# Performance work log

Measured on AMD Instinct MI355X. Metric: run time of the kernel, lower is better.

Reference implementation:

```python
import jax, jax.numpy as jnp
import numpy as np

NUM_HEADS = 6
NUM_TOKENS = 16
GROUP_SIZE = 32
PRO_COF = 0.4
CENTER_COF = 0.4


def _ln(x, g, b):
    m = jnp.mean(x, axis=-1, keepdims=True)
    v = jnp.var(x, axis=-1, keepdims=True)
    return (x - m) * jax.lax.rsqrt(v + 1e-5) * g + b


def _gelu(x):
    return jax.nn.gelu(x, approximate=False)


def _mhsa(x, qkv_w, proj_w, proj_b, mask=None):
    B, N, C = x.shape
    H = NUM_HEADS
    hd = C // H
    qkv = (x @ qkv_w.T).reshape(B, N, 3, H, hd).transpose(2, 0, 3, 1, 4)
    q, k, v = qkv[0], qkv[1], qkv[2]
    attn = jnp.einsum('bhnd,bhmd->bhnm', q, k) * (hd ** -0.5)
    if mask is not None:
        attn = attn + (mask * -100000.0)[:, None]  # additive mask, broadcast over heads
    attn = jax.nn.softmax(attn, axis=-1)
    out = jnp.einsum('bhnm,bhmd->bhnd', attn, v).transpose(0, 2, 1, 3).reshape(B, N, C)
    return out @ proj_w.T + proj_b


def _adapter(x, dw, db, uw, ub):
    # AdapterSuper: down-proj -> GELU -> up-proj + residual
    return _gelu(x @ dw.T + db) @ uw.T + ub + x


def _forward(x, mask, center1, center2, neighborhood, prompt_embeddings,
             n1_g, n1_b, qkv_w, proj_w, proj_b, n2_g, n2_b,
             fc1_w, fc1_b, fc2_w, fc2_b, ad_gate,
             ad_dw, ad_db, ad_uw, ad_ub, ad1_dw, ad1_db, ad1_uw, ad1_ub,
             bn_g, bn_b, a1_qkv_w, a1_proj_w, a1_proj_b, n3_g, n3_b,
             idx, center_idx):
    B, G1, C = x.shape
    T = NUM_TOKENS
    S = center2.shape[1]
    # mask_new: original mask in top-left, zeros for prompt slots
    mask = jnp.pad(mask, ((0, 0), (0, T), (0, T)))
    prompt = jnp.broadcast_to(prompt_embeddings[None], (B, T, C))
    x = jnp.concatenate([prompt, x], axis=1)                        # [B, T+G1, C]
    x = x + _mhsa(_ln(x, n1_g, n1_b), qkv_w, proj_w, proj_b, mask)
    h = _ln(x, n2_g, n2_b)
    x_fn = _gelu(h @ fc1_w.T + fc1_b) @ fc2_w.T + fc2_b             # MLP (drop_path=0 -> identity)
    x = ad_gate * _adapter(x_fn, ad_dw, ad_db, ad_uw, ad_ub) + x
    prompt = x[:, :T]
    xg = x[:, T:]
    prompt_x = jnp.concatenate([prompt, xg], axis=1)
    flat = prompt_x.reshape(B * (T + G1), C)
    x_neigh = flat[idx].reshape(B * S, GROUP_SIZE, C)               # irregular gather
    x_cent = flat[center_idx].reshape(B, S, C)
    # (neighborhood is normalized by its std in the original but never used afterwards)
    x_neigh = _mhsa(_ln(x_neigh, n3_g, n3_b), a1_qkv_w, a1_proj_w, a1_proj_b) + x_neigh
    knn = x_neigh.reshape(B, S, GROUP_SIZE, C)
    lc = jnp.max(knn, axis=2) + jnp.mean(knn, axis=2)               # if_maxmean=True pooling
    # eval-mode BatchNorm1d with running_mean=0, running_var=1, then GELU
    lc = _gelu(lc * bn_g * jax.lax.rsqrt(jnp.float32(1.0 + 1e-5)) + bn_b)
    vis_x = lc + CENTER_COF * x_cent                                # [B, S, C]
    # propagate: de_neighbors == S, so the sort is a no-op permutation and the
    # inverse-square-distance weighted sum runs over all centers.
    d = (jnp.sum(center1 ** 2, -1)[:, :, None] + jnp.sum(center2 ** 2, -1)[:, None, :]
         - 2.0 * jnp.einsum('bnc,bsc->bns', center1, center2))      # square_distance [B,G1,S]
    recip = 1.0 / (d + 1e-8)
    weight = recip / jnp.sum(recip, axis=-1, keepdims=True)
    interp = jnp.einsum('bns,bsc->bnc', weight, vis_x)
    new_x = xg + PRO_COF * interp
    x = jnp.concatenate([prompt, new_x], axis=1)
    x = _adapter(x, ad1_dw, ad1_db, ad1_uw, ad1_ub)
    return x[:, T:]


def setup_inputs() -> dict:
    key = jax.random.key(0)
    ks = iter(jax.random.split(key, 64))
    B, G, S, T, C, K = 32, 512, 128, NUM_TOKENS, 384, GROUP_SIZE
    H4, R = 4 * C, 16
    f32 = jnp.float32

    def rn(shape, s=0.02):
        return jax.random.normal(next(ks), shape, dtype=f32) * s

    return {
        'x': jax.random.normal(next(ks), (B, G, C), dtype=f32),
        'mask': (jax.random.uniform(next(ks), (B, G, G)) < 0.1).astype(f32),
        'center1': jax.random.normal(next(ks), (B, G, 3), dtype=f32),
        'center2': jax.random.normal(next(ks), (B, S, 3), dtype=f32),
        'neighborhood': jax.random.normal(next(ks), (B, S, K, 3), dtype=f32),
        'prompt_embeddings': rn((T, C)),
        'n1_g': jnp.ones((C,), f32), 'n1_b': jnp.zeros((C,), f32),
        'qkv_w': rn((3 * C, C)), 'proj_w': rn((C, C)), 'proj_b': jnp.zeros((C,), f32),
        'n2_g': jnp.ones((C,), f32), 'n2_b': jnp.zeros((C,), f32),
        'fc1_w': rn((H4, C)), 'fc1_b': jnp.zeros((H4,), f32),
        'fc2_w': rn((C, H4)), 'fc2_b': jnp.zeros((C,), f32),
        'ad_gate': jnp.full((1,), 0.5, f32),
        'ad_dw': rn((R, C)), 'ad_db': jnp.zeros((R,), f32),
        'ad_uw': rn((C, R)), 'ad_ub': jnp.zeros((C,), f32),
        'ad1_dw': rn((R, C)), 'ad1_db': jnp.zeros((R,), f32),
        'ad1_uw': rn((C, R)), 'ad1_ub': jnp.zeros((C,), f32),
        'bn_g': jnp.ones((C,), f32), 'bn_b': jnp.zeros((C,), f32),
        'a1_qkv_w': rn((3 * C, C)), 'a1_proj_w': rn((C, C)), 'a1_proj_b': jnp.zeros((C,), f32),
        'n3_g': jnp.ones((C,), f32), 'n3_b': jnp.zeros((C,), f32),
        'idx': jax.random.randint(next(ks), (B * S * K,), 0, B * (T + G)),
        'center_idx': jax.random.randint(next(ks), (B * S,), 0, B * (T + G)),
    }


def reference(x, mask, center1, center2, neighborhood, prompt_embeddings,
              n1_g, n1_b, qkv_w, proj_w, proj_b, n2_g, n2_b,
              fc1_w, fc1_b, fc2_w, fc2_b, ad_gate,
              ad_dw, ad_db, ad_uw, ad_ub, ad1_dw, ad1_db, ad1_uw, ad1_ub,
              bn_g, bn_b, a1_qkv_w, a1_proj_w, a1_proj_b, n3_g, n3_b,
              idx, center_idx):
    return _forward(x, mask, center1, center2, neighborhood, prompt_embeddings,
                    n1_g, n1_b, qkv_w, proj_w, proj_b, n2_g, n2_b,
                    fc1_w, fc1_b, fc2_w, fc2_b, ad_gate,
                    ad_dw, ad_db, ad_uw, ad_ub, ad1_dw, ad1_db, ad1_uw, ad1_ub,
                    bn_g, bn_b, a1_qkv_w, a1_proj_w, a1_proj_b, n3_g, n3_b,
                    idx, center_idx)
```

## Files before the change

kernel.cpp:

```cpp
#include <hip/hip_runtime.h>
#include <hip/hip_bf16.h>

#define Bq 32
#define Tq 16
#define Gq 512
#define NSEQ 528
#define Cq 384
#define Hq 6
#define Sq 128
#define Kg 32
#define ROWS (Bq*NSEQ)
#define LROWS (Bq*Sq*Kg)

typedef unsigned short u16;
typedef short bf16x8 __attribute__((ext_vector_type(8)));
typedef float f32x4  __attribute__((ext_vector_type(4)));

__device__ __forceinline__ float gelu_f(float x){
    return 0.5f * x * (1.0f + erff(x * 0.70710678118654752f));
}
__device__ __forceinline__ u16 f2b(float x){
    union { float f; unsigned u; } v; v.f = x;
    return (u16)((v.u + 0x7fffu + ((v.u >> 16) & 1u)) >> 16);
}
__device__ __forceinline__ float b2f(u16 h){
    union { float f; unsigned u; } v; v.u = ((unsigned)h) << 16; return v.f;
}

__device__ __forceinline__ void gload16(const u16* g, u16* l){
    __builtin_amdgcn_global_load_lds(
        (const __attribute__((address_space(1))) unsigned int*)(g),
        (__attribute__((address_space(3))) unsigned int*)(l), 16, 0, 0);
}

__global__ void __launch_bounds__(256) build_ln(const float* __restrict__ xin,
    const float* __restrict__ pe, const float* __restrict__ gw,
    const float* __restrict__ bw, float* __restrict__ X, u16* __restrict__ out)
{
    int w = threadIdx.x >> 6, lane = threadIdx.x & 63;
    int row = blockIdx.x*4 + w;
    if (row >= ROWS) return;
    int p = row % NSEQ; int b = row / NSEQ;
    const float* src = (p < Tq) ? (pe + (long)p*Cq)
                                : (xin + ((long)b*Gq + (p - Tq))*Cq);
    float v[6]; float s = 0.f, s2 = 0.f;
#pragma unroll
    for (int j = 0; j < 6; j++){ float x = src[lane + 64*j]; v[j] = x; s += x; s2 += x*x; }
#pragma unroll
    for (int m = 1; m < 64; m <<= 1){ s += __shfl_xor(s, m); s2 += __shfl_xor(s2, m); }
    float mean = s * (1.f/384.f);
    float var  = s2 * (1.f/384.f) - mean*mean;
    float rs   = rsqrtf(var + 1e-5f);
    float* xrow = X + (long)row*Cq;
    u16* orow = out + (long)row*Cq;
#pragma unroll
    for (int j = 0; j < 6; j++){
        int c = lane + 64*j;
        xrow[c] = v[j];
        orow[c] = f2b((v[j] - mean) * rs * gw[c] + bw[c]);
    }
}

__global__ void __launch_bounds__(256) conv6(const float* __restrict__ s0,
    const float* __restrict__ s1, const float* __restrict__ s2,
    const float* __restrict__ s3, const float* __restrict__ s4,
    const float* __restrict__ s5, u16* __restrict__ dst)
{
    long i = (long)blockIdx.x*256 + threadIdx.x;
    if (i >= 2359296) return;
    float v;
    if      (i <  442368) v = s0[i];
    else if (i <  589824) v = s1[i -  442368];
    else if (i < 1179648) v = s2[i -  589824];
    else if (i < 1769472) v = s3[i - 1179648];
    else if (i < 2211840) v = s4[i - 1769472];
    else                  v = s5[i - 2211840];
    dst[i] = f2b(v);
}

__global__ void __launch_bounds__(256) conv_mask(const float* __restrict__ m,
    u16* __restrict__ bias16)
{
    long i = (long)blockIdx.x*256 + threadIdx.x;
    if (i >= ((long)Bq*Gq*Gq >> 2)) return;
    float4 v = *(const float4*)(m + i*4);
    ushort4 r;
    r.x = f2b(-100000.0f * v.x);
    r.y = f2b(-100000.0f * v.y);
    r.z = f2b(-100000.0f * v.z);
    r.w = f2b(-100000.0f * v.w);
    *(ushort4*)(bias16 + i*4) = r;
}

__global__ void __launch_bounds__(256) ln_rows(const float* __restrict__ in,
    const float* __restrict__ gw, const float* __restrict__ bw,
    u16* __restrict__ out, int rows)
{
    int w = threadIdx.x >> 6, lane = threadIdx.x & 63;
    int row = blockIdx.x*4 + w;
    if (row >= rows) return;
    const float* xr = in + (long)row*Cq;
    float v[6]; float s = 0.f, s2 = 0.f;
#pragma unroll
    for (int j = 0; j < 6; j++){ float x = xr[lane + 64*j]; v[j] = x; s += x; s2 += x*x; }
#pragma unroll
    for (int m = 1; m < 64; m <<= 1){ s += __shfl_xor(s, m); s2 += __shfl_xor(s2, m); }
    float mean = s * (1.f/384.f);
    float var  = s2 * (1.f/384.f) - mean*mean;
    float rs   = rsqrtf(var + 1e-5f);
    u16* orow = out + (long)row*Cq;
#pragma unroll
    for (int j = 0; j < 6; j++){
        int c = lane + 64*j;
        orow[c] = f2b((v[j] - mean) * rs * gw[c] + bw[c]);
    }
}

__global__ void __launch_bounds__(512, 4) gemm_bf16(const u16* __restrict__ A,
    const u16* __restrict__ W, const float* __restrict__ bias,
    float* __restrict__ Cf, u16* __restrict__ Cb, int M, int N, int K, int epi)
{
    __shared__ u16 As0[128*32];
    __shared__ u16 As1[128*32];
    __shared__ u16 Ws0[128*32];
    __shared__ u16 Ws1[128*32];
    int t = threadIdx.x;
    int nx = gridDim.x;
    int nwg = nx * gridDim.y;
    int f = blockIdx.y*nx + blockIdx.x;
    int xcd = f & 7, i = f >> 3;
    int q = nwg >> 3, r = nwg & 7;
    int base = (xcd < r) ? xcd*(q+1) : r*(q+1) + (xcd - r)*q;
    int nf = base + i;
    int m0 = (nf / nx)*128, n0 = (nf % nx)*128;
    int wv = t >> 6, lane = t & 63;
    int wm = (wv >> 2)*64, wn = (wv & 3)*32;
    int fm = lane & 15;
    int fkp = (((lane >> 4) ^ ((fm >> 1) & 3)) & 3) * 8;
    int rs  = t >> 2;
    int kc8 = (((lane & 3) ^ ((lane >> 3) & 3))) * 8;
    f32x4 acc[4][2];
#pragma unroll
    for (int ii = 0; ii < 4; ii++)
#pragma unroll
        for (int j = 0; j < 2; j++) acc[ii][j] = (f32x4){0.f,0.f,0.f,0.f};

    auto STG = [&](u16* Ab, u16* Wb, int k0){
        gload16(A + (long)(m0 + rs)*K + k0 + kc8, Ab + wv*512);
        gload16(W + (long)(n0 + rs)*K + k0 + kc8, Wb + wv*512);
    };
    auto CMP = [&](const u16* Ab, const u16* Wb){
        bf16x8 af[4], bf[2];
#pragma unroll
        for (int im = 0; im < 4; im++) af[im] = *(const bf16x8*)&Ab[(wm + im*16 + fm)*32 + fkp];
#pragma unroll
        for (int in = 0; in < 2; in++) bf[in] = *(const bf16x8*)&Wb[(wn + in*16 + fm)*32 + fkp];
#pragma unroll
        for (int im = 0; im < 4; im++)
#pragma unroll
            for (int in = 0; in < 2; in++)
                acc[im][in] = __builtin_amdgcn_mfma_f32_16x16x32_bf16(af[im], bf[in], acc[im][in], 0, 0, 0);
    };

    int nt = K >> 5;
    STG(As0, Ws0, 0);
    __syncthreads();
    for (int kt = 0; kt < nt; kt += 2){
        STG(As1, Ws1, (kt+1)*32);
        CMP(As0, Ws0);
        __syncthreads();
        if (kt + 2 < nt) STG(As0, Ws0, (kt+2)*32);
        CMP(As1, Ws1);
        __syncthreads();
    }

    int lr = lane >> 4, lc = lane & 15;
#pragma unroll
    for (int im = 0; im < 4; im++){
#pragma unroll
        for (int in = 0; in < 2; in++){
#pragma unroll
            for (int r2 = 0; r2 < 4; r2++){
                int m = m0 + wm + im*16 + lr*4 + r2;
                int n = n0 + wn + in*16 + lc;
                float v = acc[im][in][r2];
                if (epi >= 1 && bias) v += bias[n];
                if (epi == 2) v = gelu_f(v);
                long off = (long)m*N + n;
                if (epi == 3) v += Cf[off];
                if (epi == 2 || epi == 4) Cb[off] = f2b(v);
                else                      Cf[off] = v;
            }
        }
    }
}

__global__ void __launch_bounds__(512, 4) gemm_pool(const u16* __restrict__ A,
    const u16* __restrict__ W, const float* __restrict__ bias,
    const int* __restrict__ idx, const int* __restrict__ cidx,
    const u16* __restrict__ X16, const float* __restrict__ bng,
    const float* __restrict__ bnb, float* __restrict__ vis, int K)
{
    __shared__ u16 As0[128*32];
    __shared__ u16 As1[128*32];
    __shared__ u16 Ws0[128*32];
    __shared__ u16 Ws1[128*32];
    __shared__ int idxl[128];
    __shared__ int cidxl[4];
    int t = threadIdx.x;
    int blkf = blockIdx.x;
    int xcd = blkf & 7, slot = blkf >> 3;
    int m0 = (xcd*128 + slot/3)*128;
    int n0 = (slot % 3)*128;
    if (t < 128) idxl[t] = idx[m0 + t];
    if (t < 4)   cidxl[t] = cidx[(m0 >> 5) + t];
    int wv = t >> 6, lane = t & 63;
    int wm = (wv >> 2)*64, wn = (wv & 3)*32;
    int fm = lane & 15;
    int fkp = (((lane >> 4) ^ ((fm >> 1) & 3)) & 3) * 8;
    int rs  = t >> 2;
    int kc8 = (((lane & 3) ^ ((lane >> 3) & 3))) * 8;
    f32x4 acc[4][2];
#pragma unroll
    for (int ii = 0; ii < 4; ii++)
#pragma unroll
        for (int j = 0; j < 2; j++) acc[ii][j] = (f32x4){0.f,0.f,0.f,0.f};

    auto STG = [&](u16* Ab, u16* Wb, int k0){
        gload16(A + (long)(m0 + rs)*K + k0 + kc8, Ab + wv*512);
        gload16(W + (long)(n0 + rs)*K + k0 + kc8, Wb + wv*512);
    };
    auto CMP = [&](const u16* Ab, const u16* Wb){
        bf16x8 af[4], bf[2];
#pragma unroll
        for (int im = 0; im < 4; im++) af[im] = *(const bf16x8*)&Ab[(wm + im*16 + fm)*32 + fkp];
#pragma unroll
        for (int in = 0; in < 2; in++) bf[in] = *(const bf16x8*)&Wb[(wn + in*16 + fm)*32 + fkp];
#pragma unroll
        for (int im = 0; im < 4; im++)
#pragma unroll
            for (int in = 0; in < 2; in++)
                acc[im][in] = __builtin_amdgcn_mfma_f32_16x16x32_bf16(af[im], bf[in], acc[im][in], 0, 0, 0);
    };

    int nt = K >> 5;
    STG(As0, Ws0, 0);
    __syncthreads();
    for (int kt = 0; kt < nt; kt += 2){
        STG(As1, Ws1, (kt+1)*32);
        CMP(As0, Ws0);
        __syncthreads();
        if (kt + 2 < nt) STG(As0, Ws0, (kt+2)*32);
        CMP(As1, Ws1);
        __syncthreads();
    }

    int lr = lane >> 4, lc = lane & 15;
#pragma unroll
    for (int in = 0; in < 2; in++){
        int c = n0 + wn + in*16 + lc;
        float pb = bias[c];
        float bg = bng[c], bb = bnb[c];
#pragma unroll
        for (int gl = 0; gl < 2; gl++){
            float vmax = -3e38f, vsum = 0.f;
#pragma unroll
            for (int i2 = 0; i2 < 2; i2++){
                int im = gl*2 + i2;
#pragma unroll
                for (int r = 0; r < 4; r++){
                    int rl = wm + im*16 + lr*4 + r;
                    float val = acc[im][in][r] + pb + b2f(X16[(long)idxl[rl]*Cq + c]);
                    vmax = fmaxf(vmax, val); vsum += val;
                }
            }
            vmax = fmaxf(vmax, __shfl_xor(vmax, 16)); vsum += __shfl_xor(vsum, 16);
            vmax = fmaxf(vmax, __shfl_xor(vmax, 32)); vsum += __shfl_xor(vsum, 32);
            if (lane < 16){
                int glb = (wm >> 5) + gl;
                float lcv = vmax + vsum*(1.f/32.f);
                float u = gelu_f(lcv*bg*0.9999950000374997f + bb);
                vis[((long)(m0 >> 5) + glb)*Cq + c] =
                    u + 0.4f*b2f(X16[(long)cidxl[glb]*Cq + c]);
            }
        }
    }
}

__global__ void __launch_bounds__(256) attn_mfma(const u16* __restrict__ QKVg,
    const u16* __restrict__ bias16, u16* __restrict__ out)
{
    __shared__ u16 Ks[32*72];
    __shared__ u16 Vt[64*40];
    __shared__ u16 Bs[64*36];
    __shared__ u16 Pb[4][16*40];
    int blk = blockIdx.x;
    int xcd = blk & 7; int r0 = blk >> 3;
    int bb = r0 & 3;  int rr = r0 >> 2;
    int h = rr % 6;   int qt = rr / 6;
    int b = xcd + 8*bb;
    int t = threadIdx.x; int w = t >> 6; int lane = t & 63;
    int fr  = lane & 15;
    int fko = (lane >> 4) * 8;
    int colj = lane & 15;
    int rgrp = (lane >> 4) * 4;
    int qb0 = qt*64;
    int q0 = qb0 + w*16;

    int qr = q0 + fr; int qrc = qr < NSEQ ? qr : NSEQ-1;
    const u16* qbase = QKVg + (long)(b*NSEQ + qrc)*1152 + h*64;
    bf16x8 aq0 = *(const bf16x8*)(qbase + fko);
    bf16x8 aq1 = *(const bf16x8*)(qbase + 32 + fko);

    f32x4 oacc[4];
#pragma unroll
    for (int d = 0; d < 4; d++) oacc[d] = (f32x4){0.f,0.f,0.f,0.f};
    float lsum[4] = {0.f, 0.f, 0.f, 0.f};

    int skey = t >> 3;
    int sd8  = (t & 7) * 8;
    int jswz = skey ^ ((t & 3) << 3);
    int brow = t >> 2;
    int bc8  = (t & 3) * 8;

    for (int kc = 0; kc < 17; kc++){
        __syncthreads();
        {
            int j = kc*32 + skey;
            bf16x8 kv = {0,0,0,0,0,0,0,0};
            bf16x8 vv = {0,0,0,0,0,0,0,0};
            if (j < NSEQ){
                const u16* kb = QKVg + (long)(b*NSEQ + j)*1152 + 384 + h*64 + sd8;
                kv = *(const bf16x8*)kb;
                vv = *(const bf16x8*)(kb + 384);
            }
            *(bf16x8*)&Ks[skey*72 + sd8] = kv;
#pragma unroll
            for (int e = 0; e < 8; e++) Vt[(sd8+e)*40 + jswz] = (u16)vv[e];
        }
        {
            int qi = qb0 + brow;
            int jj = kc*32 + bc8;
            uint4 bz = make_uint4(0u,0u,0u,0u);
            if (qi < Gq && jj < Gq)
                bz = *(const uint4*)(bias16 + ((long)b*Gq + qi)*Gq + jj);
            *(uint4*)&Bs[brow*36 + bc8] = bz;
        }
        __syncthreads();
        f32x4 s[2];
#pragma unroll
        for (int sub = 0; sub < 2; sub++){
            bf16x8 bk0 = *(const bf16x8*)&Ks[(sub*16 + fr)*72 + fko];
            bf16x8 bk1 = *(const bf16x8*)&Ks[(sub*16 + fr)*72 + 32 + fko];
            f32x4 z = (f32x4){0.f,0.f,0.f,0.f};
            z = __builtin_amdgcn_mfma_f32_16x16x32_bf16(aq0, bk0, z, 0, 0, 0);
            z = __builtin_amdgcn_mfma_f32_16x16x32_bf16(aq1, bk1, z, 0, 0, 0);
            s[sub] = z;
        }
#pragma unroll
        for (int sub = 0; sub < 2; sub++){
#pragma unroll
            for (int r = 0; r < 4; r++){
                int jj = kc*32 + sub*16 + colj;
                float sv = s[sub][r] * 0.125f
                         + b2f(Bs[(w*16 + rgrp + r)*36 + sub*16 + colj]);
                if (jj >= NSEQ) sv = -1e30f;
                float e = __expf(sv);
                lsum[r] += e;
                Pb[w][(rgrp + r)*40 + sub*16 + colj] = f2b(e);
            }
        }
        __syncthreads();
        bf16x8 ap = *(const bf16x8*)&Pb[w][fr*40 + fko];
#pragma unroll
        for (int d = 0; d < 4; d++){
            int D = d*16 + fr;
            int fkv = fko ^ (((D >> 3) & 3) << 3);
            bf16x8 bv = *(const bf16x8*)&Vt[D*40 + fkv];
            oacc[d] = __builtin_amdgcn_mfma_f32_16x16x32_bf16(ap, bv, oacc[d], 0, 0, 0);
        }
    }
#pragma unroll
    for (int r = 0; r < 4; r++){
#pragma unroll
        for (int mm = 1; mm < 16; mm <<= 1) lsum[r] += __shfl_xor(lsum[r], mm);
    }
#pragma unroll
    for (int r = 0; r < 4; r++){
        int qi = q0 + rgrp + r;
        if (qi < NSEQ){
            float inv = 1.0f / lsum[r];
#pragma unroll
            for (int d = 0; d < 4; d++)
                out[((long)(b*NSEQ + qi))*Cq + h*64 + d*16 + colj] = f2b(oacc[d][r]*inv);
        }
    }
}

__global__ void __launch_bounds__(256) adapter_fused(const float* __restrict__ xfn,
    const float* __restrict__ resid,
    const float* __restrict__ dw, const float* __restrict__ db,
    const float* __restrict__ uw, const float* __restrict__ ub,
    const float* __restrict__ gatep,
    const float* __restrict__ lng, const float* __restrict__ lnb,
    float* __restrict__ Xout, u16* __restrict__ x16out,
    u16* __restrict__ ln16, int rows)
{
    int w = threadIdx.x >> 6, lane = threadIdx.x & 63;
    int row = blockIdx.x*4 + w;
    if (row >= rows) return;
    const float* xr = xfn + (long)row*Cq;
    float xv[6];
#pragma unroll
    for (int j = 0; j < 6; j++) xv[j] = xr[lane + 64*j];
    float hid[16];
#pragma unroll
    for (int r = 0; r < 16; r++){
        const float* dr = dw + r*Cq;
        float p = 0.f;
#pragma unroll
        for (int j = 0; j < 6; j++) p += xv[j]*dr[lane + 64*j];
#pragma unroll
        for (int mm = 1; mm < 64; mm <<= 1) p += __shfl_xor(p, mm);
        hid[r] = gelu_f(p + db[r]);
    }
    float gate = gatep ? gatep[0] : 1.0f;
    float ov[6];
    float s = 0.f, s2 = 0.f;
#pragma unroll
    for (int j = 0; j < 6; j++){
        int c = lane + 64*j;
        const float* uc = uw + c*16;
        float a = 0.f;
#pragma unroll
        for (int r = 0; r < 16; r++) a += hid[r]*uc[r];
        float v = gate * (a + ub[c] + xv[j]);
        if (resid) v += resid[(long)row*Cq + c];
        ov[j] = v;
        Xout[(long)row*Cq + c] = v;
        if (x16out) x16out[(long)row*Cq + c] = f2b(v);
        s += v; s2 += v*v;
    }
    if (lng){
#pragma unroll
        for (int m = 1; m < 64; m <<= 1){ s += __shfl_xor(s, m); s2 += __shfl_xor(s2, m); }
        float mean = s * (1.f/384.f);
        float var  = s2 * (1.f/384.f) - mean*mean;
        float rs   = rsqrtf(var + 1e-5f);
        u16* orow = ln16 + (long)row*Cq;
#pragma unroll
        for (int j = 0; j < 6; j++){
            int c = lane + 64*j;
            orow[c] = f2b((ov[j] - mean)*rs*lng[c] + lnb[c]);
        }
    }
}

__global__ void __launch_bounds__(256) local_attn(const u16* __restrict__ QKVg,
    const int* __restrict__ idx, u16* __restrict__ aout16)
{
    __shared__ u16 Qs[32*72];
    __shared__ u16 Ksm[32*72];
    __shared__ u16 Vt[64*40];
    __shared__ float sc[32*36];
    __shared__ u16 Pa[32*40];
    __shared__ float linv[32];
    __shared__ int rows[32];
    int g = blockIdx.x;
    int t = threadIdx.x;
    int w = t >> 6, lane = t & 63;
    if (t < 32) rows[t] = idx[g*Kg + t];
    __syncthreads();
    int srow = t & 31;
    int d8   = (t >> 5) * 8;
    int jswz = srow ^ (((t >> 5) & 3) << 3);
    int fr = lane & 15, fko = (lane >> 4)*8;
    int colj = lane & 15, rgrp = (lane >> 4)*4;
    int it = w >> 1, jt = w & 1;
    int smrow = w*8 + (lane >> 3);
    int smc   = (lane & 7) * 4;

    for (int h = 0; h < Hq; h++){
        {
            const u16* base = QKVg + (long)rows[srow]*1152 + h*64 + d8;
            bf16x8 qv = *(const bf16x8*)(base);
            bf16x8 kv = *(const bf16x8*)(base + 384);
            bf16x8 vv = *(const bf16x8*)(base + 768);
            *(bf16x8*)&Qs[srow*72 + d8]  = qv;
            *(bf16x8*)&Ksm[srow*72 + d8] = kv;
#pragma unroll
            for (int e = 0; e < 8; e++) Vt[(d8+e)*40 + jswz] = (u16)vv[e];
        }
        __syncthreads();
        {
            bf16x8 a0 = *(const bf16x8*)&Qs[(it*16+fr)*72 + fko];
            bf16x8 a1 = *(const bf16x8*)&Qs[(it*16+fr)*72 + 32 + fko];
            bf16x8 b0 = *(const bf16x8*)&Ksm[(jt*16+fr)*72 + fko];
            bf16x8 b1 = *(const bf16x8*)&Ksm[(jt*16+fr)*72 + 32 + fko];
            f32x4 z = (f32x4){0.f,0.f,0.f,0.f};
            z = __builtin_amdgcn_mfma_f32_16x16x32_bf16(a0, b0, z, 0, 0, 0);
            z = __builtin_amdgcn_mfma_f32_16x16x32_bf16(a1, b1, z, 0, 0, 0);
#pragma unroll
            for (int r = 0; r < 4; r++)
                sc[(it*16 + rgrp + r)*36 + jt*16 + colj] = z[r]*0.125f;
        }
        __syncthreads();
        {
            float4 s4 = *(const float4*)&sc[smrow*36 + smc];
            float mx = fmaxf(fmaxf(s4.x, s4.y), fmaxf(s4.z, s4.w));
#pragma unroll
            for (int mm = 1; mm < 8; mm <<= 1) mx = fmaxf(mx, __shfl_xor(mx, mm));
            float p0 = __expf(s4.x - mx), p1 = __expf(s4.y - mx);
            float p2 = __expf(s4.z - mx), p3 = __expf(s4.w - mx);
            float sm = p0 + p1 + p2 + p3;
#pragma unroll
            for (int mm = 1; mm < 8; mm <<= 1) sm += __shfl_xor(sm, mm);
            if ((lane & 7) == 0) linv[smrow] = 1.0f / sm;
            Pa[smrow*40 + smc + 0] = f2b(p0);
            Pa[smrow*40 + smc + 1] = f2b(p1);
            Pa[smrow*40 + smc + 2] = f2b(p2);
            Pa[smrow*40 + smc + 3] = f2b(p3);
        }
        __syncthreads();
        {
            bf16x8 ap = *(const bf16x8*)&Pa[(it*16+fr)*40 + fko];
#pragma unroll
            for (int dd = 0; dd < 2; dd++){
                int dt = jt + dd*2;
                int D = dt*16 + fr;
                int fkv = fko ^ (((D >> 3) & 3) << 3);
                bf16x8 bv = *(const bf16x8*)&Vt[D*40 + fkv];
                f32x4 o = (f32x4){0.f,0.f,0.f,0.f};
                o = __builtin_amdgcn_mfma_f32_16x16x32_bf16(ap, bv, o, 0, 0, 0);
#pragma unroll
                for (int r = 0; r < 4; r++){
                    int row = it*16 + rgrp + r;
                    aout16[((long)(g*32 + row))*Cq + h*64 + dt*16 + colj] =
                        f2b(o[r] * linv[row]);
                }
            }
        }
        __syncthreads();
    }
}

__global__ void __launch_bounds__(128) interp_k(const float* __restrict__ Xf,
    const float* __restrict__ vis, const float* __restrict__ c1,
    const float* __restrict__ c2, float* __restrict__ newx)
{
    __shared__ float wsh[8*128];
    __shared__ float inv8[8];
    int blk = blockIdx.x;
    int b = blk >> 6, nt = blk & 63;
    int tid = threadIdx.x;
#pragma unroll
    for (int i = 0; i < 8; i++){
        int id = tid + i*128;
        int nl = id >> 7, s = id & 127;
        const float* p1 = c1 + ((long)b*Gq + nt*8 + nl)*3;
        const float* p2 = c2 + ((long)b*Sq + s)*3;
        float x1 = p1[0], y1 = p1[1], z1 = p1[2];
        float x2 = p2[0], y2 = p2[1], z2 = p2[2];
        float d = (x1*x1 + y1*y1 + z1*z1) + (x2*x2 + y2*y2 + z2*z2)
                - 2.f*(x1*x2 + y1*y2 + z1*z2);
        wsh[nl*128 + s] = 1.f/(d + 1e-8f);
    }
    __syncthreads();
    if (tid < 8){
        float sum = 0.f;
        for (int s = 0; s < Sq; s++) sum += wsh[tid*128 + s];
        inv8[tid] = 1.f/sum;
    }
    __syncthreads();
    float acc[8][3];
#pragma unroll
    for (int n = 0; n < 8; n++){ acc[n][0] = 0.f; acc[n][1] = 0.f; acc[n][2] = 0.f; }
    const float* vb = vis + (long)b*Sq*Cq + tid;
    for (int s = 0; s < Sq; s++){
        float v0 = vb[s*Cq], v1 = vb[s*Cq + 128], v2 = vb[s*Cq + 256];
#pragma unroll
        for (int n = 0; n < 8; n++){
            float wq = wsh[n*128 + s];
            acc[n][0] += wq*v0; acc[n][1] += wq*v1; acc[n][2] += wq*v2;
        }
    }
#pragma unroll
    for (int n = 0; n < 8; n++){
        int gn = nt*8 + n;
        const float* xr = Xf + ((long)(b*NSEQ + Tq + gn))*Cq;
        float* orow = newx + ((long)(b*Gq + gn))*Cq;
        float sf = 0.4f * inv8[n];
        orow[tid]       = xr[tid]       + sf*acc[n][0];
        orow[tid + 128] = xr[tid + 128] + sf*acc[n][1];
        orow[tid + 256] = xr[tid + 256] + sf*acc[n][2];
    }
}

extern "C" void kernel_launch(void* const* d_in, const int* in_sizes, int n_in,
                              void* d_out, int out_size, void* d_ws, size_t ws_size,
                              hipStream_t stream)
{
    const float* x_in  = (const float*)d_in[0];
    const float* mask  = (const float*)d_in[1];
    const float* c1p   = (const float*)d_in[2];
    const float* c2p   = (const float*)d_in[3];
    const float* pe    = (const float*)d_in[5];
    const float* n1g   = (const float*)d_in[6];
    const float* n1b   = (const float*)d_in[7];
    const float* qkvw  = (const float*)d_in[8];
    const float* projw = (const float*)d_in[9];
    const float* projb = (const float*)d_in[10];
    const float* n2g   = (const float*)d_in[11];
    const float* n2b   = (const float*)d_in[12];
    const float* fc1w  = (const float*)d_in[13];
    const float* fc1b  = (const float*)d_in[14];
    const float* fc2w  = (const float*)d_in[15];
    const float* fc2b  = (const float*)d_in[16];
    const float* gate  = (const float*)d_in[17];
    const float* addw  = (const float*)d_in[18];
    const float* addb  = (const float*)d_in[19];
    const float* aduw  = (const float*)d_in[20];
    const float* adub  = (const float*)d_in[21];
    const float* ad1dw = (const float*)d_in[22];
    const float* ad1db = (const float*)d_in[23];
    const float* ad1uw = (const float*)d_in[24];
    const float* ad1ub = (const float*)d_in[25];
    const float* bng   = (const float*)d_in[26];
    const float* bnb   = (const float*)d_in[27];
    const float* a1qkvw= (const float*)d_in[28];
    const float* a1pw  = (const float*)d_in[29];
    const float* a1pb  = (const float*)d_in[30];
    const float* n3g   = (const float*)d_in[31];
    const float* n3b   = (const float*)d_in[32];
    const int*   idxp  = (const int*)d_in[33];
    const int*   cidxp = (const int*)d_in[34];

    char* w = (char*)d_ws;
    float* X    = (float*)w;
    u16*   WB   = (u16*)(w + 25952256);
    u16*   Bb16 = (u16*)(w + 30670848);
    char*  R1   = w + 43646976;
    char*  R2   = R1 + 100663296;
    float* V    = (float*)(R2 + 100663296);

    u16* qkvw16  = WB;
    u16* projw16 = WB +  442368;
    u16* fc1w16  = WB +  589824;
    u16* fc2w16  = WB + 1179648;
    u16* a1qkv16 = WB + 1769472;
    u16* a1pw16  = WB + 2211840;

    u16*   bias16 = (u16*)R1;
    u16*   hid16  = (u16*)R1;
    u16*   aout16 = (u16*)R1;
    u16*   QKVg   = (u16*)R2;
    float* C1     = (float*)R2;
    float* newx   = (float*)R2;
    u16*   X16    = (u16*)(R2 + 41943040);

    conv6<<<9216, 256, 0, stream>>>(qkvw, projw, fc1w, fc2w, a1qkvw, a1pw, WB);
    conv_mask<<<8192, 256, 0, stream>>>(mask, bias16);
    build_ln<<<4224, 256, 0, stream>>>(x_in, pe, n1g, n1b, X, Bb16);
    gemm_bf16<<<dim3(9, 132), 512, 0, stream>>>(Bb16, qkvw16, nullptr, nullptr, QKVg,
                                                ROWS, 1152, Cq, 4);
    attn_mfma<<<1728, 256, 0, stream>>>(QKVg, bias16, Bb16);
    gemm_bf16<<<dim3(3, 132), 512, 0, stream>>>(Bb16, projw16, projb, X, nullptr,
                                                ROWS, Cq, Cq, 3);
    ln_rows<<<4224, 256, 0, stream>>>(X, n2g, n2b, Bb16, ROWS);
    gemm_bf16<<<dim3(12, 132), 512, 0, stream>>>(Bb16, fc1w16, fc1b, nullptr, hid16,
                                                 ROWS, 1536, Cq, 2);
    gemm_bf16<<<dim3(3, 132), 512, 0, stream>>>(hid16, fc2w16, fc2b, C1, nullptr,
                                                ROWS, Cq, 1536, 1);
    adapter_fused<<<4224, 256, 0, stream>>>(C1, X, addw, addb, aduw, adub, gate,
                                            n3g, n3b, X, X16, Bb16, ROWS);
    gemm_bf16<<<dim3(9, 132), 512, 0, stream>>>(Bb16, a1qkv16, nullptr, nullptr, QKVg,
                                                ROWS, 1152, Cq, 4);
    local_attn<<<4096, 256, 0, stream>>>(QKVg, idxp, aout16);
    gemm_pool<<<3072, 512, 0, stream>>>(aout16, a1pw16, a1pb, idxp, cidxp,
                                        X16, bng, bnb, V, Cq);
    interp_k<<<2048, 128, 0, stream>>>(X, V, c1p, c2p, newx);
    adapter_fused<<<4096, 256, 0, stream>>>(newx, nullptr, ad1dw, ad1db, ad1uw, ad1ub,
                                            nullptr, nullptr, nullptr,
                                            (float*)d_out, nullptr, nullptr, Bq*Gq);
}
```

Measured before the change: 689.1 us.

## Deepen GEMM LDS pipeline to four stages with vmcnt-based barriers

```diff
diff --git a/kernel.cpp b/kernel.cpp
--- a/kernel.cpp
+++ b/kernel.cpp
@@ -33,6 +33,12 @@
         (__attribute__((address_space(3))) unsigned int*)(l), 16, 0, 0);
 }
 
+#define PIPE_BAR(N) do { \
+    asm volatile("s_waitcnt vmcnt(" #N ")" ::: "memory"); \
+    __builtin_amdgcn_s_barrier(); \
+    __builtin_amdgcn_sched_barrier(0); \
+} while(0)
+
 __global__ void __launch_bounds__(256) build_ln(const float* __restrict__ xin,
     const float* __restrict__ pe, const float* __restrict__ gw,
     const float* __restrict__ bw, float* __restrict__ X, u16* __restrict__ out)
@@ -122,8 +128,12 @@
 {
     __shared__ u16 As0[128*32];
     __shared__ u16 As1[128*32];
+    __shared__ u16 As2[128*32];
+    __shared__ u16 As3[128*32];
     __shared__ u16 Ws0[128*32];
     __shared__ u16 Ws1[128*32];
+    __shared__ u16 Ws2[128*32];
+    __shared__ u16 Ws3[128*32];
     int t = threadIdx.x;
     int nx = gridDim.x;
     int nwg = nx * gridDim.y;
@@ -164,15 +174,17 @@
 
     int nt = K >> 5;
     STG(As0, Ws0, 0);
-    __syncthreads();
-    for (int kt = 0; kt < nt; kt += 2){
-        STG(As1, Ws1, (kt+1)*32);
-        CMP(As0, Ws0);
-        __syncthreads();
-        if (kt + 2 < nt) STG(As0, Ws0, (kt+2)*32);
-        CMP(As1, Ws1);
-        __syncthreads();
-    }
+    STG(As1, Ws1, 32);
+    for (int g = 0; g + 4 < nt; g += 4){
+        STG(As2, Ws2, (g+2)*32); PIPE_BAR(4); CMP(As0, Ws0);
+        STG(As3, Ws3, (g+3)*32); PIPE_BAR(4); CMP(As1, Ws1);
+        STG(As0, Ws0, (g+4)*32); PIPE_BAR(4); CMP(As2, Ws2);
+        STG(As1, Ws1, (g+5)*32); PIPE_BAR(4); CMP(As3, Ws3);
+    }
+    STG(As2, Ws2, (nt-2)*32); PIPE_BAR(4); CMP(As0, Ws0);
+    STG(As3, Ws3, (nt-1)*32); PIPE_BAR(4); CMP(As1, Ws1);
+    PIPE_BAR(2); CMP(As2, Ws2);
+    PIPE_BAR(0); CMP(As3, Ws3);
 
     int lr = lane >> 4, lc = lane & 15;
 #pragma unroll
@@ -203,8 +215,12 @@
 {
     __shared__ u16 As0[128*32];
     __shared__ u16 As1[128*32];
+    __shared__ u16 As2[128*32];
+    __shared__ u16 As3[128*32];
     __shared__ u16 Ws0[128*32];
     __shared__ u16 Ws1[128*32];
+    __shared__ u16 Ws2[128*32];
+    __shared__ u16 Ws3[128*32];
     __shared__ int idxl[128];
     __shared__ int cidxl[4];
     int t = threadIdx.x;
@@ -245,15 +261,17 @@
 
     int nt = K >> 5;
     STG(As0, Ws0, 0);
-    __syncthreads();
-    for (int kt = 0; kt < nt; kt += 2){
-        STG(As1, Ws1, (kt+1)*32);
-        CMP(As0, Ws0);
-        __syncthreads();
-        if (kt + 2 < nt) STG(As0, Ws0, (kt+2)*32);
-        CMP(As1, Ws1);
-        __syncthreads();
-    }
+    STG(As1, Ws1, 32);
+    for (int g = 0; g + 4 < nt; g += 4){
+        STG(As2, Ws2, (g+2)*32); PIPE_BAR(4); CMP(As0, Ws0);
+        STG(As3, Ws3, (g+3)*32); PIPE_BAR(4); CMP(As1, Ws1);
+        STG(As0, Ws0, (g+4)*32); PIPE_BAR(4); CMP(As2, Ws2);
+        STG(As1, Ws1, (g+5)*32); PIPE_BAR(4); CMP(As3, Ws3);
+    }
+    STG(As2, Ws2, (nt-2)*32); PIPE_BAR(4); CMP(As0, Ws0);
+    STG(As3, Ws3, (nt-1)*32); PIPE_BAR(4); CMP(As1, Ws1);
+    PIPE_BAR(2); CMP(As2, Ws2);
+    PIPE_BAR(0); CMP(As3, Ws3);
 
     int lr = lane >> 4, lc = lane & 15;
 #pragma unroll
```

Measured after the change: 693.9 us. No clear change (+0.7%).

## Merge prep kernels and register-prefetch next tiles in attention kernels

Applied to the files above, without the earlier changes.

```diff
diff --git a/kernel.cpp b/kernel.cpp
--- a/kernel.cpp
+++ b/kernel.cpp
@@ -33,63 +33,65 @@
         (__attribute__((address_space(3))) unsigned int*)(l), 16, 0, 0);
 }
 
-__global__ void __launch_bounds__(256) build_ln(const float* __restrict__ xin,
-    const float* __restrict__ pe, const float* __restrict__ gw,
-    const float* __restrict__ bw, float* __restrict__ X, u16* __restrict__ out)
-{
-    int w = threadIdx.x >> 6, lane = threadIdx.x & 63;
-    int row = blockIdx.x*4 + w;
-    if (row >= ROWS) return;
-    int p = row % NSEQ; int b = row / NSEQ;
-    const float* src = (p < Tq) ? (pe + (long)p*Cq)
-                                : (xin + ((long)b*Gq + (p - Tq))*Cq);
-    float v[6]; float s = 0.f, s2 = 0.f;
-#pragma unroll
-    for (int j = 0; j < 6; j++){ float x = src[lane + 64*j]; v[j] = x; s += x; s2 += x*x; }
-#pragma unroll
-    for (int m = 1; m < 64; m <<= 1){ s += __shfl_xor(s, m); s2 += __shfl_xor(s2, m); }
-    float mean = s * (1.f/384.f);
-    float var  = s2 * (1.f/384.f) - mean*mean;
-    float rs   = rsqrtf(var + 1e-5f);
-    float* xrow = X + (long)row*Cq;
-    u16* orow = out + (long)row*Cq;
-#pragma unroll
-    for (int j = 0; j < 6; j++){
-        int c = lane + 64*j;
-        xrow[c] = v[j];
-        orow[c] = f2b((v[j] - mean) * rs * gw[c] + bw[c]);
-    }
-}
-
-__global__ void __launch_bounds__(256) conv6(const float* __restrict__ s0,
-    const float* __restrict__ s1, const float* __restrict__ s2,
-    const float* __restrict__ s3, const float* __restrict__ s4,
-    const float* __restrict__ s5, u16* __restrict__ dst)
-{
-    long i = (long)blockIdx.x*256 + threadIdx.x;
-    if (i >= 2359296) return;
-    float v;
-    if      (i <  442368) v = s0[i];
-    else if (i <  589824) v = s1[i -  442368];
-    else if (i < 1179648) v = s2[i -  589824];
-    else if (i < 1769472) v = s3[i - 1179648];
-    else if (i < 2211840) v = s4[i - 1769472];
-    else                  v = s5[i - 2211840];
-    dst[i] = f2b(v);
-}
-
-__global__ void __launch_bounds__(256) conv_mask(const float* __restrict__ m,
-    u16* __restrict__ bias16)
-{
-    long i = (long)blockIdx.x*256 + threadIdx.x;
-    if (i >= ((long)Bq*Gq*Gq >> 2)) return;
-    float4 v = *(const float4*)(m + i*4);
-    ushort4 r;
-    r.x = f2b(-100000.0f * v.x);
-    r.y = f2b(-100000.0f * v.y);
-    r.z = f2b(-100000.0f * v.z);
-    r.w = f2b(-100000.0f * v.w);
-    *(ushort4*)(bias16 + i*4) = r;
+__global__ void __launch_bounds__(256) prep(const float* __restrict__ qkvw,
+    const float* __restrict__ projw, const float* __restrict__ fc1w,
+    const float* __restrict__ fc2w, const float* __restrict__ a1qkvw,
+    const float* __restrict__ a1pw, u16* __restrict__ WB,
+    const float* __restrict__ mask, u16* __restrict__ bias16,
+    const float* __restrict__ xin, const float* __restrict__ pe,
+    const float* __restrict__ gw, const float* __restrict__ bw,
+    float* __restrict__ X, u16* __restrict__ out)
+{
+    int bid = blockIdx.x;
+    if (bid < 9216){
+        long i = (long)bid*256 + threadIdx.x;
+        if (i >= 2359296) return;
+        float v;
+        if      (i <  442368) v = qkvw[i];
+        else if (i <  589824) v = projw[i -  442368];
+        else if (i < 1179648) v = fc1w[i -  589824];
+        else if (i < 1769472) v = fc2w[i - 1179648];
+        else if (i < 2211840) v = a1qkvw[i - 1769472];
+        else                  v = a1pw[i - 2211840];
+        WB[i] = f2b(v);
+        return;
+    }
+    if (bid < 17408){
+        long i = (long)(bid - 9216)*256 + threadIdx.x;
+        if (i >= ((long)Bq*Gq*Gq >> 2)) return;
+        float4 v = *(const float4*)(mask + i*4);
+        ushort4 r;
+        r.x = f2b(-100000.0f * v.x);
+        r.y = f2b(-100000.0f * v.y);
+        r.z = f2b(-100000.0f * v.z);
+        r.w = f2b(-100000.0f * v.w);
+        *(ushort4*)(bias16 + i*4) = r;
+        return;
+    }
+    {
+        int w = threadIdx.x >> 6, lane = threadIdx.x & 63;
+        int row = (bid - 17408)*4 + w;
+        if (row >= ROWS) return;
+        int p = row % NSEQ; int b = row / NSEQ;
+        const float* src = (p < Tq) ? (pe + (long)p*Cq)
+                                    : (xin + ((long)b*Gq + (p - Tq))*Cq);
+        float v[6]; float s = 0.f, s2 = 0.f;
+#pragma unroll
+        for (int j = 0; j < 6; j++){ float x = src[lane + 64*j]; v[j] = x; s += x; s2 += x*x; }
+#pragma unroll
+        for (int m = 1; m < 64; m <<= 1){ s += __shfl_xor(s, m); s2 += __shfl_xor(s2, m); }
+        float mean = s * (1.f/384.f);
+        float var  = s2 * (1.f/384.f) - mean*mean;
+        float rs   = rsqrtf(var + 1e-5f);
+        float* xrow = X + (long)row*Cq;
+        u16* orow = out + (long)row*Cq;
+#pragma unroll
+        for (int j = 0; j < 6; j++){
+            int c = lane + 64*j;
+            xrow[c] = v[j];
+            orow[c] = f2b((v[j] - mean) * rs * gw[c] + bw[c]);
+        }
+    }
 }
 
 __global__ void __launch_bounds__(256) ln_rows(const float* __restrict__ in,
@@ -323,30 +325,35 @@
     int brow = t >> 2;
     int bc8  = (t & 3) * 8;
 
+    bf16x8 kvR = {0,0,0,0,0,0,0,0}, vvR = {0,0,0,0,0,0,0,0};
+    uint4  bzR = make_uint4(0u,0u,0u,0u);
+    auto LD = [&](int kc){
+        int j = kc*32 + skey;
+        bf16x8 kv = {0,0,0,0,0,0,0,0};
+        bf16x8 vv = {0,0,0,0,0,0,0,0};
+        if (j < NSEQ){
+            const u16* kb = QKVg + (long)(b*NSEQ + j)*1152 + 384 + h*64 + sd8;
+            kv = *(const bf16x8*)kb;
+            vv = *(const bf16x8*)(kb + 384);
+        }
+        int qi = qb0 + brow;
+        int jj = kc*32 + bc8;
+        uint4 bz = make_uint4(0u,0u,0u,0u);
+        if (qi < Gq && jj < Gq)
+            bz = *(const uint4*)(bias16 + ((long)b*Gq + qi)*Gq + jj);
+        kvR = kv; vvR = vv; bzR = bz;
+    };
+    LD(0);
+
     for (int kc = 0; kc < 17; kc++){
         __syncthreads();
-        {
-            int j = kc*32 + skey;
-            bf16x8 kv = {0,0,0,0,0,0,0,0};
-            bf16x8 vv = {0,0,0,0,0,0,0,0};
-            if (j < NSEQ){
-                const u16* kb = QKVg + (long)(b*NSEQ + j)*1152 + 384 + h*64 + sd8;
-                kv = *(const bf16x8*)kb;
-                vv = *(const bf16x8*)(kb + 384);
-            }
-            *(bf16x8*)&Ks[skey*72 + sd8] = kv;
-#pragma unroll
-            for (int e = 0; e < 8; e++) Vt[(sd8+e)*40 + jswz] = (u16)vv[e];
-        }
-        {
-            int qi = qb0 + brow;
-            int jj = kc*32 + bc8;
-            uint4 bz = make_uint4(0u,0u,0u,0u);
-            if (qi < Gq && jj < Gq)
-                bz = *(const uint4*)(bias16 + ((long)b*Gq + qi)*Gq + jj);
-            *(uint4*)&Bs[brow*36 + bc8] = bz;
-        }
-        __syncthreads();
+        *(bf16x8*)&Ks[skey*72 + sd8] = kvR;
+#pragma unroll
+        for (int e = 0; e < 8; e++) Vt[(sd8+e)*40 + jswz] = (u16)kvR[e], Vt[(sd8+e)*40 + jswz] = (u16)vvR[e];
+        *(uint4*)&Bs[brow*36 + bc8] = bzR;
+        if (kc < 16) LD(kc + 1);
+        __syncthreads();
+
         f32x4 s[2];
 #pragma unroll
         for (int sub = 0; sub < 2; sub++){
@@ -370,7 +377,6 @@
                 Pb[w][(rgrp + r)*40 + sub*16 + colj] = f2b(e);
             }
         }
-        __syncthreads();
         bf16x8 ap = *(const bf16x8*)&Pb[w][fr*40 + fko];
 #pragma unroll
         for (int d = 0; d < 4; d++){
@@ -480,16 +486,21 @@
     int smrow = w*8 + (lane >> 3);
     int smc   = (lane & 7) * 4;
 
+    const u16* rbase = QKVg + (long)rows[srow]*1152 + d8;
+    bf16x8 qvR = *(const bf16x8*)(rbase);
+    bf16x8 kvR = *(const bf16x8*)(rbase + 384);
+    bf16x8 vvR = *(const bf16x8*)(rbase + 768);
+
     for (int h = 0; h < Hq; h++){
-        {
-            const u16* base = QKVg + (long)rows[srow]*1152 + h*64 + d8;
-            bf16x8 qv = *(const bf16x8*)(base);
-            bf16x8 kv = *(const bf16x8*)(base + 384);
-            bf16x8 vv = *(const bf16x8*)(base + 768);
-            *(bf16x8*)&Qs[srow*72 + d8]  = qv;
-            *(bf16x8*)&Ksm[srow*72 + d8] = kv;
-#pragma unroll
-            for (int e = 0; e < 8; e++) Vt[(d8+e)*40 + jswz] = (u16)vv[e];
+        *(bf16x8*)&Qs[srow*72 + d8]  = qvR;
+        *(bf16x8*)&Ksm[srow*72 + d8] = kvR;
+#pragma unroll
+        for (int e = 0; e < 8; e++) Vt[(d8+e)*40 + jswz] = (u16)vvR[e];
+        if (h < Hq-1){
+            const u16* nb = rbase + (h+1)*64;
+            qvR = *(const bf16x8*)(nb);
+            kvR = *(const bf16x8*)(nb + 384);
+            vvR = *(const bf16x8*)(nb + 768);
         }
         __syncthreads();
         {
@@ -658,9 +669,8 @@
     float* newx   = (float*)R2;
     u16*   X16    = (u16*)(R2 + 41943040);
 
-    conv6<<<9216, 256, 0, stream>>>(qkvw, projw, fc1w, fc2w, a1qkvw, a1pw, WB);
-    conv_mask<<<8192, 256, 0, stream>>>(mask, bias16);
-    build_ln<<<4224, 256, 0, stream>>>(x_in, pe, n1g, n1b, X, Bb16);
+    prep<<<21632, 256, 0, stream>>>(qkvw, projw, fc1w, fc2w, a1qkvw, a1pw, WB,
+                                    mask, bias16, x_in, pe, n1g, n1b, X, Bb16);
     gemm_bf16<<<dim3(9, 132), 512, 0, stream>>>(Bb16, qkvw16, nullptr, nullptr, QKVg,
                                                 ROWS, 1152, Cq, 4);
     attn_mfma<<<1728, 256, 0, stream>>>(QKVg, bias16, Bb16);
```

Result: no change. 683.3 us (-0.8%).
